# Kernel tuning notes

Hardware: AMD Instinct MI355X
Metric: run time of the kernel (lower is better)

The kernel has to match this reference:

```python
import jax, jax.numpy as jnp
import numpy as np

DIM = 1024
HEADS = 16
DIM_HEAD = DIM // HEADS  # 64
B, N = 4, 1024


def setup_inputs() -> dict:
    key = jax.random.key(0)
    ks = jax.random.split(key, 8)
    s = 1.0 / np.sqrt(DIM)
    inp = {
        "x": jax.random.normal(ks[0], (B, N, DIM), dtype=jnp.float32),
        # weights stored as [in, out] so y = x @ W (+ b), equivalent to torch Linear
        "Wq": jax.random.normal(ks[1], (DIM, DIM), dtype=jnp.float32) * s,
        "Wk": jax.random.normal(ks[2], (DIM, DIM), dtype=jnp.float32) * s,
        "Wv": jax.random.normal(ks[3], (DIM, DIM), dtype=jnp.float32) * s,
        "Wproj": jax.random.normal(ks[4], (DIM, DIM), dtype=jnp.float32) * s,
        "bproj": jnp.zeros((DIM,), dtype=jnp.float32),
        "Wpre": jax.random.normal(ks[5], (DIM, DIM), dtype=jnp.float32) * s,
        "bpre": jnp.zeros((DIM,), dtype=jnp.float32),
        # original init is -inf (non-runnable); use a finite trained value
        "pi": jnp.full((1,), 0.5, dtype=jnp.float32),
    }
    return inp


def reference(x, Wq, Wk, Wv, Wproj, bproj, Wpre, bpre, pi):
    b, n, c = x.shape
    h, dh = HEADS, DIM_HEAD
    residual = x
    # bias-logit path: Linear -> SiLU -> bmm with itself (dropout p=0 is identity)
    pre = jax.nn.silu(x @ Wpre + bpre)                       # [B,N,C]
    logits = jnp.einsum('bnc,bmc->bnm', pre, pre) / jnp.sqrt(jnp.float32(c))
    # QKV (x2 defaults to x)
    q = (x @ Wq).reshape(b, n, h, dh).transpose(0, 2, 1, 3)  # [B,H,N,Dh]
    k = (x @ Wk).reshape(b, n, h, dh).transpose(0, 2, 1, 3)
    v = (x @ Wv).reshape(b, n, h, dh).transpose(0, 2, 1, 3)
    score = jnp.einsum('bhnd,bhmd->bhnm', q, k) / jnp.sqrt(jnp.float32(dh))
    final_logits = pi[0] * logits[:, None, :, :] + score     # broadcast bias over heads
    attn = jax.nn.softmax(final_logits, axis=-1)
    out = jnp.einsum('bhnm,bhmd->bhnd', attn, v)             # [B,H,N,Dh]
    out = out.transpose(0, 2, 1, 3).reshape(b, n, h * dh)
    out = out @ Wproj + bproj
    return out + residual
```

## Files before the change

### kernel.cpp

```cpp
#include <hip/hip_runtime.h>

using bf16x8 = __attribute__((ext_vector_type(8))) short;
using v8bf   = __attribute__((ext_vector_type(8))) __bf16;
using f32x4  = __attribute__((ext_vector_type(4))) float;

typedef const __attribute__((address_space(1))) void GASV;
typedef __attribute__((address_space(3))) void LASV;

template <typename V>
__device__ __forceinline__ auto mfma_bf16_impl(V a, V b, f32x4 c, int)
    -> decltype(__builtin_amdgcn_mfma_f32_16x16x32_bf16(a, b, c, 0, 0, 0)) {
  return __builtin_amdgcn_mfma_f32_16x16x32_bf16(a, b, c, 0, 0, 0);
}
template <typename V>
__device__ __forceinline__ f32x4 mfma_bf16_impl(V a, V b, f32x4 c, long) {
  return __builtin_amdgcn_mfma_f32_16x16x32_bf16(
      __builtin_bit_cast(v8bf, a), __builtin_bit_cast(v8bf, b), c, 0, 0, 0);
}
__device__ __forceinline__ f32x4 MFMA(bf16x8 a, bf16x8 b, f32x4 c) {
  return mfma_bf16_impl(a, b, c, 0);
}

__device__ __forceinline__ void async_lds16(const void* g, void* l) {
  __builtin_amdgcn_global_load_lds((GASV*)g, (LASV*)l, 16, 0, 0);
}

__device__ __forceinline__ unsigned short f2bf(float x) {
  unsigned u = __float_as_uint(x);
  u = u + 0x7fffu + ((u >> 16) & 1u);
  return (unsigned short)(u >> 16);
}
__device__ __forceinline__ float bf2f(unsigned short s) {
  return __uint_as_float(((unsigned)s) << 16);
}

#define LOG2E 1.4426950408889634f

__global__ __launch_bounds__(256) void k_cvt_x(const float4* __restrict__ x,
                                               ushort4* __restrict__ o) {
  int i = blockIdx.x * 256 + threadIdx.x;
  float4 v = x[i];
  ushort4 p;
  p.x = f2bf(v.x); p.y = f2bf(v.y); p.z = f2bf(v.z); p.w = f2bf(v.w);
  o[i] = p;
}

__global__ __launch_bounds__(256) void k_transpose_w(
    const float* __restrict__ w0, const float* __restrict__ w1,
    const float* __restrict__ w2, const float* __restrict__ w3,
    const float* __restrict__ w4, unsigned short* __restrict__ out) {
  __shared__ float t[32][33];
  const int z = blockIdx.z;
  const float* W = (z == 0) ? w0 : (z == 1) ? w1 : (z == 2) ? w2 : (z == 3) ? w3 : w4;
  unsigned short* o = out + (size_t)z * (1u << 20);
  const int bx = blockIdx.x * 32, by = blockIdx.y * 32;
  const int tx = threadIdx.x, ty = threadIdx.y;
#pragma unroll
  for (int i = 0; i < 4; ++i)
    t[ty + i * 8][tx] = W[(size_t)(by + ty + i * 8) * 1024 + bx + tx];
  __syncthreads();
#pragma unroll
  for (int i = 0; i < 4; ++i)
    o[(size_t)(bx + ty + i * 8) * 1024 + by + tx] = f2bf(t[tx][ty + i * 8]);
}

template <int MI, int NI>
__device__ __forceinline__ void gemm_core_t(const unsigned short* __restrict__ A,
                                            const unsigned short* __restrict__ Bt,
                                            unsigned short* ldsA,
                                            unsigned short* ldsB,
                                            f32x4 acc[MI][NI]) {
  const int tid = threadIdx.x;
  const int w = tid >> 6, lane = tid & 63;
  const int lane15 = lane & 15, quad = lane >> 4;
  const int wm = w >> 1, wn = w & 1;
  for (int ko = 0; ko < 32; ++ko) {
    __syncthreads();
#pragma unroll
    for (int i = 0; i < MI / 2; ++i) {
      const int p = i * 256 + tid;
      async_lds16(A + (p >> 2) * 1024 + ko * 32 + (p & 3) * 8,
                  ldsA + (i * 256 + w * 64) * 8);
    }
#pragma unroll
    for (int i = 0; i < NI / 2; ++i) {
      const int p = i * 256 + tid;
      async_lds16(Bt + (p >> 2) * 1024 + ko * 32 + (p & 3) * 8,
                  ldsB + (i * 256 + w * 64) * 8);
    }
    __syncthreads();
    bf16x8 af[MI], bfr[NI];
#pragma unroll
    for (int t = 0; t < MI; ++t)
      af[t] = *(const bf16x8*)&ldsA[(wm * (MI * 16) + t * 16 + lane15) * 32 + quad * 8];
#pragma unroll
    for (int t = 0; t < NI; ++t)
      bfr[t] = *(const bf16x8*)&ldsB[(wn * (NI * 16) + t * 16 + lane15) * 32 + quad * 8];
#pragma unroll
    for (int mi = 0; mi < MI; ++mi)
#pragma unroll
      for (int ni = 0; ni < NI; ++ni)
        acc[mi][ni] = MFMA(af[mi], bfr[ni], acc[mi][ni]);
  }
}

#define GEMM_PROLOGUE(MI_, NI_)                                      \
  __shared__ unsigned short ldsA[(MI_)*32 * 32];                     \
  __shared__ unsigned short ldsB[(NI_)*32 * 32];                     \
  f32x4 acc[MI_][NI_];                                               \
  {                                                                  \
    f32x4 z_ = {0.f, 0.f, 0.f, 0.f};                                 \
    for (int i_ = 0; i_ < (MI_); ++i_)                               \
      for (int j_ = 0; j_ < (NI_); ++j_) acc[i_][j_] = z_;           \
  }

#define GEMM_EPI_IDX(MI_, NI_)                                       \
  const int tid = threadIdx.x, w = tid >> 6, lane = tid & 63;        \
  const int lane15 = lane & 15, quad = lane >> 4;                    \
  const int wm = w >> 1, wn = w & 1;                                 \
  const int r0 = tm + wm * ((MI_)*16) + quad * 4;                    \
  const int c0 = tn + wn * ((NI_)*16) + lane15;

__global__ __launch_bounds__(256) void k_gemm_qkvpre(
    const unsigned short* __restrict__ xb, const unsigned short* __restrict__ wt,
    const float* __restrict__ bpre, unsigned short* __restrict__ pre,
    unsigned short* __restrict__ qb, unsigned short* __restrict__ kb,
    unsigned short* __restrict__ vt) {
  const int z = blockIdx.z;
  const int tm = blockIdx.y * 128, tn = blockIdx.x * 128;
  GEMM_PROLOGUE(4, 4);
  gemm_core_t<4, 4>(xb + (size_t)tm * 1024,
                    wt + (size_t)z * (1u << 20) + (size_t)tn * 1024, ldsA, ldsB, acc);
  GEMM_EPI_IDX(4, 4);
  if (z == 0) {
#pragma unroll
    for (int mi = 0; mi < 4; ++mi)
#pragma unroll
      for (int ni = 0; ni < 4; ++ni) {
        const int cg = c0 + ni * 16;
        const float bb = bpre[cg];
#pragma unroll
        for (int rr = 0; rr < 4; ++rr) {
          const int m = r0 + mi * 16 + rr;
          float v = acc[mi][ni][rr] + bb;
          v = v / (1.0f + __expf(-v));
          pre[(size_t)m * 1024 + cg] = f2bf(v);
        }
      }
  } else if (z == 1) {
#pragma unroll
    for (int mi = 0; mi < 4; ++mi)
#pragma unroll
      for (int ni = 0; ni < 4; ++ni) {
        const int cg = c0 + ni * 16;
#pragma unroll
        for (int rr = 0; rr < 4; ++rr)
          qb[(size_t)(r0 + mi * 16 + rr) * 1024 + cg] =
              f2bf(acc[mi][ni][rr] * (LOG2E / 8.0f));
      }
  } else if (z == 2) {
#pragma unroll
    for (int mi = 0; mi < 4; ++mi)
#pragma unroll
      for (int ni = 0; ni < 4; ++ni) {
        const int cg = c0 + ni * 16;
#pragma unroll
        for (int rr = 0; rr < 4; ++rr)
          kb[(size_t)(r0 + mi * 16 + rr) * 1024 + cg] = f2bf(acc[mi][ni][rr]);
      }
  } else {
#pragma unroll
    for (int mi = 0; mi < 4; ++mi) {
      const int m = r0 + mi * 16;
      const int bb_ = m >> 10, nseq = m & 1023;
#pragma unroll
      for (int ni = 0; ni < 4; ++ni) {
        const int cg = c0 + ni * 16;
        const int hh = cg >> 6, dd = cg & 63;
        ushort4 pk;
        pk.x = f2bf(acc[mi][ni][0]); pk.y = f2bf(acc[mi][ni][1]);
        pk.z = f2bf(acc[mi][ni][2]); pk.w = f2bf(acc[mi][ni][3]);
        *(ushort4*)&vt[(size_t)(((bb_ * 16 + hh) << 6) + dd) * 1024 + nseq] = pk;
      }
    }
  }
}

__global__ __launch_bounds__(256) void k_gemm_logits(
    const unsigned short* __restrict__ pre, const float* __restrict__ pi,
    unsigned short* __restrict__ lg) {
  const int bz = blockIdx.z;
  const unsigned short* base = pre + ((size_t)bz << 20);
  const int tm = blockIdx.y * 64, tn = blockIdx.x * 128;
  GEMM_PROLOGUE(2, 4);
  gemm_core_t<2, 4>(base + (size_t)tm * 1024, base + (size_t)tn * 1024, ldsA, ldsB, acc);
  const float sc = pi[0] * (LOG2E / 32.0f);
  GEMM_EPI_IDX(2, 4);
#pragma unroll
  for (int mi = 0; mi < 2; ++mi)
#pragma unroll
    for (int ni = 0; ni < 4; ++ni) {
      const int cg = c0 + ni * 16;
#pragma unroll
      for (int rr = 0; rr < 4; ++rr)
        lg[((size_t)bz << 20) + (size_t)(r0 + mi * 16 + rr) * 1024 + cg] =
            f2bf(acc[mi][ni][rr] * sc);
    }
}

__global__ __launch_bounds__(256) void k_gemm_out(
    const unsigned short* __restrict__ ao, const unsigned short* __restrict__ wtp,
    const float* __restrict__ bproj, const float* __restrict__ xres,
    float* __restrict__ out) {
  const int tm = blockIdx.y * 64, tn = blockIdx.x * 128;
  GEMM_PROLOGUE(2, 4);
  gemm_core_t<2, 4>(ao + (size_t)tm * 1024, wtp + (size_t)tn * 1024, ldsA, ldsB, acc);
  GEMM_EPI_IDX(2, 4);
#pragma unroll
  for (int mi = 0; mi < 2; ++mi)
#pragma unroll
    for (int ni = 0; ni < 4; ++ni) {
      const int cg = c0 + ni * 16;
      const float bb = bproj[cg];
#pragma unroll
      for (int rr = 0; rr < 4; ++rr) {
        const size_t idx = (size_t)(r0 + mi * 16 + rr) * 1024 + cg;
        out[idx] = acc[mi][ni][rr] + bb + xres[idx];
      }
    }
}

__global__ __launch_bounds__(256, 3) void k_attn(
    const unsigned short* __restrict__ qb, const unsigned short* __restrict__ kb,
    const unsigned short* __restrict__ vt, const unsigned short* __restrict__ lg,
    unsigned short* __restrict__ ao) {
  __shared__ unsigned short ldsK[128 * 64];
  __shared__ unsigned short ldsV[64 * 128];
  __shared__ unsigned short ldsP[4][16 * 128];
  const int b = blockIdx.z, h = blockIdx.y, q0 = blockIdx.x * 64;
  const int tid = threadIdx.x, w = tid >> 6, lane = tid & 63;
  const int lane15 = lane & 15, quad = lane >> 4;
  const int qw = q0 + w * 16;
  char* Pb = (char*)&ldsP[w][0];

  bf16x8 qf[2];
  {
    const unsigned short* qrow =
        qb + (size_t)((b << 10) + qw + lane15) * 1024 + (h << 6);
    qf[0] = *(const bf16x8*)(qrow + quad * 8);
    qf[1] = *(const bf16x8*)(qrow + 32 + quad * 8);
  }
  float mcol = -__builtin_inff(), lcol = 0.f;
  f32x4 o[4];
  {
    f32x4 z_ = {0.f, 0.f, 0.f, 0.f};
#pragma unroll
    for (int nt = 0; nt < 4; ++nt) o[nt] = z_;
  }

  for (int c = 0; c < 8; ++c) {
    const int kv0 = c * 128;
    __syncthreads();
#pragma unroll
    for (int i = 0; i < 4; ++i) {
      const int p = i * 256 + tid;
      {
        const int r = p >> 3, cc = (p & 7) ^ (r & 7);
        async_lds16(kb + (size_t)((b << 10) + kv0 + r) * 1024 + (h << 6) + cc * 8,
                    ldsK + (i * 256 + w * 64) * 8);
      }
      {
        const int r = p >> 4, cc = (p & 15) ^ (r & 15);
        async_lds16(vt + (size_t)(((b * 16 + h) << 6) + r) * 1024 + kv0 + cc * 8,
                    ldsV + (i * 256 + w * 64) * 8);
      }
    }
    uint2 lgv[8];
    {
      const unsigned short* lgrow =
          lg + ((size_t)b << 20) + (size_t)(qw + lane15) * 1024 + kv0 + quad * 4;
#pragma unroll
      for (int mi = 0; mi < 8; ++mi) lgv[mi] = *(const uint2*)(lgrow + mi * 16);
    }
    __syncthreads();

    f32x4 s[8];
#pragma unroll
    for (int mi = 0; mi < 8; ++mi) {
      const int row = mi * 16 + lane15;
      bf16x8 k0 = *(const bf16x8*)&ldsK[row * 64 + ((quad ^ (row & 7)) << 3)];
      bf16x8 k1 = *(const bf16x8*)&ldsK[row * 64 + (((4 + quad) ^ (row & 7)) << 3)];
      f32x4 t = {0.f, 0.f, 0.f, 0.f};
      t = MFMA(k0, qf[0], t);
      t = MFMA(k1, qf[1], t);
      s[mi] = t;
    }
#pragma unroll
    for (int mi = 0; mi < 8; ++mi) {
      s[mi][0] += __uint_as_float(lgv[mi].x << 16);
      s[mi][1] += __uint_as_float(lgv[mi].x & 0xffff0000u);
      s[mi][2] += __uint_as_float(lgv[mi].y << 16);
      s[mi][3] += __uint_as_float(lgv[mi].y & 0xffff0000u);
    }
    float mx = s[0][0];
#pragma unroll
    for (int mi = 0; mi < 8; ++mi)
#pragma unroll
      for (int rr = 0; rr < 4; ++rr) mx = fmaxf(mx, s[mi][rr]);
    mx = fmaxf(mx, __shfl_xor(mx, 16));
    mx = fmaxf(mx, __shfl_xor(mx, 32));
    const float mn = fmaxf(mcol, mx);
    const float al = exp2f(mcol - mn);
    mcol = mn;
    float rs = 0.f;
#pragma unroll
    for (int mi = 0; mi < 8; ++mi) {
      const float p0 = exp2f(s[mi][0] - mn), p1 = exp2f(s[mi][1] - mn);
      const float p2 = exp2f(s[mi][2] - mn), p3 = exp2f(s[mi][3] - mn);
      rs += (p0 + p1) + (p2 + p3);
      const unsigned dw0 = ((__float_as_uint(p1) + 0x8000u) & 0xffff0000u) |
                           ((__float_as_uint(p0) + 0x8000u) >> 16);
      const unsigned dw1 = ((__float_as_uint(p3) + 0x8000u) & 0xffff0000u) |
                           ((__float_as_uint(p2) + 0x8000u) >> 16);
      *(uint2*)(Pb + lane15 * 256 + (((2 * mi + (quad >> 1)) ^ lane15) << 4) +
                ((quad & 1) << 3)) = make_uint2(dw0, dw1);
    }
    rs += __shfl_xor(rs, 16);
    rs += __shfl_xor(rs, 32);
    lcol = lcol * al + rs;
    float ar[4];
#pragma unroll
    for (int rr = 0; rr < 4; ++rr) ar[rr] = __shfl(al, quad * 4 + rr);
#pragma unroll
    for (int nt = 0; nt < 4; ++nt)
#pragma unroll
      for (int rr = 0; rr < 4; ++rr) o[nt][rr] *= ar[rr];
#pragma unroll
    for (int ks = 0; ks < 4; ++ks) {
      bf16x8 pf = *(const bf16x8*)(Pb + lane15 * 256 +
                                   ((((ks << 2) + quad) ^ lane15) << 4));
#pragma unroll
      for (int nt = 0; nt < 4; ++nt) {
        const int d = nt * 16 + lane15;
        bf16x8 vf = *(const bf16x8*)&ldsV[d * 128 +
                                          (((ks * 4 + quad) ^ (d & 15)) << 3)];
        o[nt] = MFMA(pf, vf, o[nt]);
      }
    }
  }
  const float rinv = 1.0f / lcol;
  float rv[4];
#pragma unroll
  for (int rr = 0; rr < 4; ++rr) rv[rr] = __shfl(rinv, quad * 4 + rr);
#pragma unroll
  for (int nt = 0; nt < 4; ++nt) {
    const int cg = (h << 6) + nt * 16 + lane15;
#pragma unroll
    for (int rr = 0; rr < 4; ++rr) {
      const int m = (b << 10) + qw + quad * 4 + rr;
      ao[(size_t)m * 1024 + cg] = f2bf(o[nt][rr] * rv[rr]);
    }
  }
}

extern "C" void kernel_launch(void* const* d_in, const int* in_sizes, int n_in,
                              void* d_out, int out_size, void* d_ws, size_t ws_size,
                              hipStream_t stream) {
  const float* x     = (const float*)d_in[0];
  const float* Wq    = (const float*)d_in[1];
  const float* Wk    = (const float*)d_in[2];
  const float* Wv    = (const float*)d_in[3];
  const float* Wproj = (const float*)d_in[4];
  const float* bproj = (const float*)d_in[5];
  const float* Wpre  = (const float*)d_in[6];
  const float* bpre  = (const float*)d_in[7];
  const float* pi    = (const float*)d_in[8];
  float* out = (float*)d_out;
  char* ws = (char*)d_ws;

  unsigned short* xb  = (unsigned short*)(ws);
  unsigned short* wt  = (unsigned short*)(ws + (8u << 20));
  unsigned short* pre = (unsigned short*)(ws + (18u << 20));
  unsigned short* qb  = (unsigned short*)(ws + (26u << 20));
  unsigned short* kb  = (unsigned short*)(ws + (34u << 20));
  unsigned short* vt  = (unsigned short*)(ws + (42u << 20));
  unsigned short* lg  = xb;
  unsigned short* ao  = pre;

  k_cvt_x<<<dim3(4096), dim3(256), 0, stream>>>((const float4*)x, (ushort4*)xb);
  k_transpose_w<<<dim3(32, 32, 5), dim3(32, 8), 0, stream>>>(Wpre, Wq, Wk, Wv, Wproj, wt);
  k_gemm_qkvpre<<<dim3(8, 32, 4), dim3(256), 0, stream>>>(xb, wt, bpre, pre, qb, kb, vt);
  k_gemm_logits<<<dim3(8, 16, 4), dim3(256), 0, stream>>>(pre, pi, lg);
  k_attn<<<dim3(16, 16, 4), dim3(256), 0, stream>>>(qb, kb, vt, lg, ao);
  k_gemm_out<<<dim3(8, 64, 1), dim3(256), 0, stream>>>(ao, wt + 4 * (1u << 20), bproj, x, out);
}
```

Measured before the change: 247.4 us.

## Swap GEMM operands for vectorized epilogue stores and alias attention P buffer into K LDS

The QKV/pre, logits and output GEMMs now compute the transposed product (weights as the A operand), so each lane's four accumulator rows are contiguous in memory and can be written as ushort4/float4 vector stores instead of scalar strided stores. The bias load becomes a float4, and the residual read and output write are vectorized. In attention, the logit bias is loaded into the MFMA accumulator as its initial value rather than added afterwards. The per-wave P buffer now reuses the K LDS region behind an extra barrier, cutting LDS use so occupancy can rise (launch bound 3 to 5), at the cost of an additional __syncthreads per tile and the risk of register spills.

Measured after the change: 280.4 us. 13.3% more time.

```diff
diff --git a/kernel.cpp b/kernel.cpp
--- a/kernel.cpp
+++ b/kernel.cpp
@@ -29,9 +29,6 @@
   unsigned u = __float_as_uint(x);
   u = u + 0x7fffu + ((u >> 16) & 1u);
   return (unsigned short)(u >> 16);
-}
-__device__ __forceinline__ float bf2f(unsigned short s) {
-  return __uint_as_float(((unsigned)s) << 16);
 }
 
 #define LOG2E 1.4426950408889634f
@@ -127,46 +124,60 @@
     unsigned short* __restrict__ qb, unsigned short* __restrict__ kb,
     unsigned short* __restrict__ vt) {
   const int z = blockIdx.z;
-  const int tm = blockIdx.y * 128, tn = blockIdx.x * 128;
+  int tm, tn;
+  if (z == 3) { tm = blockIdx.y * 128; tn = blockIdx.x * 128; }
+  else        { tm = blockIdx.x * 128; tn = blockIdx.y * 128; }
+  const unsigned short* At =
+      (z == 3) ? xb + (size_t)tm * 1024
+               : wt + (size_t)z * (1u << 20) + (size_t)tm * 1024;
+  const unsigned short* Bt_ =
+      (z == 3) ? wt + (size_t)3 * (1u << 20) + (size_t)tn * 1024
+               : xb + (size_t)tn * 1024;
   GEMM_PROLOGUE(4, 4);
-  gemm_core_t<4, 4>(xb + (size_t)tm * 1024,
-                    wt + (size_t)z * (1u << 20) + (size_t)tn * 1024, ldsA, ldsB, acc);
+  gemm_core_t<4, 4>(At, Bt_, ldsA, ldsB, acc);
   GEMM_EPI_IDX(4, 4);
   if (z == 0) {
 #pragma unroll
+    for (int mi = 0; mi < 4; ++mi) {
+      const float4 b4 = *(const float4*)&bpre[r0 + mi * 16];
+#pragma unroll
+      for (int ni = 0; ni < 4; ++ni) {
+        const int seq = c0 + ni * 16;
+        float vv[4];
+#pragma unroll
+        for (int rr = 0; rr < 4; ++rr) {
+          float v = acc[mi][ni][rr] + ((const float*)&b4)[rr];
+          vv[rr] = v / (1.0f + __expf(-v));
+        }
+        ushort4 pk;
+        pk.x = f2bf(vv[0]); pk.y = f2bf(vv[1]);
+        pk.z = f2bf(vv[2]); pk.w = f2bf(vv[3]);
+        *(ushort4*)&pre[(size_t)seq * 1024 + r0 + mi * 16] = pk;
+      }
+    }
+  } else if (z == 1) {
+#pragma unroll
     for (int mi = 0; mi < 4; ++mi)
 #pragma unroll
       for (int ni = 0; ni < 4; ++ni) {
-        const int cg = c0 + ni * 16;
-        const float bb = bpre[cg];
-#pragma unroll
-        for (int rr = 0; rr < 4; ++rr) {
-          const int m = r0 + mi * 16 + rr;
-          float v = acc[mi][ni][rr] + bb;
-          v = v / (1.0f + __expf(-v));
-          pre[(size_t)m * 1024 + cg] = f2bf(v);
-        }
-      }
-  } else if (z == 1) {
+        const int seq = c0 + ni * 16;
+        ushort4 pk;
+        pk.x = f2bf(acc[mi][ni][0] * (LOG2E / 8.0f));
+        pk.y = f2bf(acc[mi][ni][1] * (LOG2E / 8.0f));
+        pk.z = f2bf(acc[mi][ni][2] * (LOG2E / 8.0f));
+        pk.w = f2bf(acc[mi][ni][3] * (LOG2E / 8.0f));
+        *(ushort4*)&qb[(size_t)seq * 1024 + r0 + mi * 16] = pk;
+      }
+  } else if (z == 2) {
 #pragma unroll
     for (int mi = 0; mi < 4; ++mi)
 #pragma unroll
       for (int ni = 0; ni < 4; ++ni) {
-        const int cg = c0 + ni * 16;
-#pragma unroll
-        for (int rr = 0; rr < 4; ++rr)
-          qb[(size_t)(r0 + mi * 16 + rr) * 1024 + cg] =
-              f2bf(acc[mi][ni][rr] * (LOG2E / 8.0f));
-      }
-  } else if (z == 2) {
-#pragma unroll
-    for (int mi = 0; mi < 4; ++mi)
-#pragma unroll
-      for (int ni = 0; ni < 4; ++ni) {
-        const int cg = c0 + ni * 16;
-#pragma unroll
-        for (int rr = 0; rr < 4; ++rr)
-          kb[(size_t)(r0 + mi * 16 + rr) * 1024 + cg] = f2bf(acc[mi][ni][rr]);
+        const int seq = c0 + ni * 16;
+        ushort4 pk;
+        pk.x = f2bf(acc[mi][ni][0]); pk.y = f2bf(acc[mi][ni][1]);
+        pk.z = f2bf(acc[mi][ni][2]); pk.w = f2bf(acc[mi][ni][3]);
+        *(ushort4*)&kb[(size_t)seq * 1024 + r0 + mi * 16] = pk;
       }
   } else {
 #pragma unroll
@@ -200,11 +211,11 @@
   for (int mi = 0; mi < 2; ++mi)
 #pragma unroll
     for (int ni = 0; ni < 4; ++ni) {
-      const int cg = c0 + ni * 16;
-#pragma unroll
-      for (int rr = 0; rr < 4; ++rr)
-        lg[((size_t)bz << 20) + (size_t)(r0 + mi * 16 + rr) * 1024 + cg] =
-            f2bf(acc[mi][ni][rr] * sc);
+      const int col = c0 + ni * 16;
+      ushort4 pk;
+      pk.x = f2bf(acc[mi][ni][0] * sc); pk.y = f2bf(acc[mi][ni][1] * sc);
+      pk.z = f2bf(acc[mi][ni][2] * sc); pk.w = f2bf(acc[mi][ni][3] * sc);
+      *(ushort4*)&lg[((size_t)bz << 20) + (size_t)col * 1024 + r0 + mi * 16] = pk;
     }
 }
 
@@ -212,36 +223,39 @@
     const unsigned short* __restrict__ ao, const unsigned short* __restrict__ wtp,
     const float* __restrict__ bproj, const float* __restrict__ xres,
     float* __restrict__ out) {
-  const int tm = blockIdx.y * 64, tn = blockIdx.x * 128;
+  const int tm = blockIdx.x * 64, tn = blockIdx.y * 128;
   GEMM_PROLOGUE(2, 4);
-  gemm_core_t<2, 4>(ao + (size_t)tm * 1024, wtp + (size_t)tn * 1024, ldsA, ldsB, acc);
+  gemm_core_t<2, 4>(wtp + (size_t)tm * 1024, ao + (size_t)tn * 1024, ldsA, ldsB, acc);
   GEMM_EPI_IDX(2, 4);
 #pragma unroll
-  for (int mi = 0; mi < 2; ++mi)
+  for (int mi = 0; mi < 2; ++mi) {
+    const float4 b4 = *(const float4*)&bproj[r0 + mi * 16];
 #pragma unroll
     for (int ni = 0; ni < 4; ++ni) {
-      const int cg = c0 + ni * 16;
-      const float bb = bproj[cg];
-#pragma unroll
-      for (int rr = 0; rr < 4; ++rr) {
-        const size_t idx = (size_t)(r0 + mi * 16 + rr) * 1024 + cg;
-        out[idx] = acc[mi][ni][rr] + bb + xres[idx];
-      }
-    }
-}
-
-__global__ __launch_bounds__(256, 3) void k_attn(
+      const int seq = c0 + ni * 16;
+      const size_t idx = (size_t)seq * 1024 + r0 + mi * 16;
+      const float4 rv = *(const float4*)&xres[idx];
+      float4 ov;
+      ov.x = acc[mi][ni][0] + b4.x + rv.x;
+      ov.y = acc[mi][ni][1] + b4.y + rv.y;
+      ov.z = acc[mi][ni][2] + b4.z + rv.z;
+      ov.w = acc[mi][ni][3] + b4.w + rv.w;
+      *(float4*)&out[idx] = ov;
+    }
+  }
+}
+
+__global__ __launch_bounds__(256, 5) void k_attn(
     const unsigned short* __restrict__ qb, const unsigned short* __restrict__ kb,
     const unsigned short* __restrict__ vt, const unsigned short* __restrict__ lg,
     unsigned short* __restrict__ ao) {
   __shared__ unsigned short ldsK[128 * 64];
   __shared__ unsigned short ldsV[64 * 128];
-  __shared__ unsigned short ldsP[4][16 * 128];
   const int b = blockIdx.z, h = blockIdx.y, q0 = blockIdx.x * 64;
   const int tid = threadIdx.x, w = tid >> 6, lane = tid & 63;
   const int lane15 = lane & 15, quad = lane >> 4;
   const int qw = q0 + w * 16;
-  char* Pb = (char*)&ldsP[w][0];
+  char* Pb = (char*)(ldsK + w * 2048);
 
   bf16x8 qf[2];
   {
@@ -290,17 +304,14 @@
       const int row = mi * 16 + lane15;
       bf16x8 k0 = *(const bf16x8*)&ldsK[row * 64 + ((quad ^ (row & 7)) << 3)];
       bf16x8 k1 = *(const bf16x8*)&ldsK[row * 64 + (((4 + quad) ^ (row & 7)) << 3)];
-      f32x4 t = {0.f, 0.f, 0.f, 0.f};
+      f32x4 t;
+      t[0] = __uint_as_float(lgv[mi].x << 16);
+      t[1] = __uint_as_float(lgv[mi].x & 0xffff0000u);
+      t[2] = __uint_as_float(lgv[mi].y << 16);
+      t[3] = __uint_as_float(lgv[mi].y & 0xffff0000u);
       t = MFMA(k0, qf[0], t);
       t = MFMA(k1, qf[1], t);
       s[mi] = t;
-    }
-#pragma unroll
-    for (int mi = 0; mi < 8; ++mi) {
-      s[mi][0] += __uint_as_float(lgv[mi].x << 16);
-      s[mi][1] += __uint_as_float(lgv[mi].x & 0xffff0000u);
-      s[mi][2] += __uint_as_float(lgv[mi].y << 16);
-      s[mi][3] += __uint_as_float(lgv[mi].y & 0xffff0000u);
     }
     float mx = s[0][0];
 #pragma unroll
@@ -313,17 +324,16 @@
     const float al = exp2f(mcol - mn);
     mcol = mn;
     float rs = 0.f;
+    uint2 pk[8];
 #pragma unroll
     for (int mi = 0; mi < 8; ++mi) {
       const float p0 = exp2f(s[mi][0] - mn), p1 = exp2f(s[mi][1] - mn);
       const float p2 = exp2f(s[mi][2] - mn), p3 = exp2f(s[mi][3] - mn);
       rs += (p0 + p1) + (p2 + p3);
-      const unsigned dw0 = ((__float_as_uint(p1) + 0x8000u) & 0xffff0000u) |
-                           ((__float_as_uint(p0) + 0x8000u) >> 16);
-      const unsigned dw1 = ((__float_as_uint(p3) + 0x8000u) & 0xffff0000u) |
-                           ((__float_as_uint(p2) + 0x8000u) >> 16);
-      *(uint2*)(Pb + lane15 * 256 + (((2 * mi + (quad >> 1)) ^ lane15) << 4) +
-                ((quad & 1) << 3)) = make_uint2(dw0, dw1);
+      pk[mi].x = ((__float_as_uint(p1) + 0x8000u) & 0xffff0000u) |
+                 ((__float_as_uint(p0) + 0x8000u) >> 16);
+      pk[mi].y = ((__float_as_uint(p3) + 0x8000u) & 0xffff0000u) |
+                 ((__float_as_uint(p2) + 0x8000u) >> 16);
     }
     rs += __shfl_xor(rs, 16);
     rs += __shfl_xor(rs, 32);
@@ -335,6 +345,12 @@
     for (int nt = 0; nt < 4; ++nt)
 #pragma unroll
       for (int rr = 0; rr < 4; ++rr) o[nt][rr] *= ar[rr];
+
+    __syncthreads();
+#pragma unroll
+    for (int mi = 0; mi < 8; ++mi)
+      *(uint2*)(Pb + lane15 * 256 + (((2 * mi + (quad >> 1)) ^ lane15) << 4) +
+                ((quad & 1) << 3)) = pk[mi];
 #pragma unroll
     for (int ks = 0; ks < 4; ++ks) {
       bf16x8 pf = *(const bf16x8*)(Pb + lane15 * 256 +
@@ -392,5 +408,5 @@
   k_gemm_qkvpre<<<dim3(8, 32, 4), dim3(256), 0, stream>>>(xb, wt, bpre, pre, qb, kb, vt);
   k_gemm_logits<<<dim3(8, 16, 4), dim3(256), 0, stream>>>(pre, pi, lg);
   k_attn<<<dim3(16, 16, 4), dim3(256), 0, stream>>>(qb, kb, vt, lg, ao);
-  k_gemm_out<<<dim3(8, 64, 1), dim3(256), 0, stream>>>(ao, wt + 4 * (1u << 20), bproj, x, out);
-}
+  k_gemm_out<<<dim3(16, 32, 1), dim3(256), 0, stream>>>(ao, wt + 4 * (1u << 20), bproj, x, out);
+}
```
